# Performance work log

Hardware: AMD Instinct MI355X
Metric: run time of the kernel (lower is better)

Reference implementation:

```python
import jax, jax.numpy as jnp
import numpy as np

N_GRAPHS = 256
RATIO = 0.5


def setup_inputs() -> dict:
    key = jax.random.key(0)
    k0, k1, k2, k3, k4 = jax.random.split(key, 5)
    N, E, D = 100000, 1600000, 64
    x = jax.random.normal(k0, (N, D), dtype=jnp.float32)
    edge_index = jax.random.randint(k1, (2, E), 0, N, dtype=jnp.int32)
    batch = jnp.sort(jax.random.randint(k2, (N,), 0, N_GRAPHS, dtype=jnp.int32))
    # GraphConv(in_channels=64, out_channels=1) parameters
    w_rel = jax.random.normal(k3, (D,), dtype=jnp.float32) * 0.1
    b_rel = jnp.zeros((), dtype=jnp.float32)
    w_root = jax.random.normal(k4, (D,), dtype=jnp.float32) * 0.1
    return {"x": x, "edge_index": edge_index, "batch": batch,
            "w_rel": w_rel, "b_rel": b_rel, "w_root": w_root}


def reference(x, edge_index, batch, w_rel, b_rel, w_root):
    N = x.shape[0]
    src, dst = edge_index[0], edge_index[1]
    # GraphConv score: lin_rel(sum_{j in N(i)} x_j) + lin_root(x_i)
    agg = jax.ops.segment_sum(x[src], dst, num_segments=N)        # [N, D]
    score = jnp.tanh(agg @ w_rel + b_rel + x @ w_root)            # [N], SAGPool tanh
    # per-graph topk: keep k_g = ceil(ratio * n_g) highest-score nodes
    sizes = jax.ops.segment_sum(jnp.ones(N, jnp.int32), batch,
                                num_segments=N_GRAPHS)            # [G]
    k = jnp.ceil(RATIO * sizes.astype(jnp.float32)).astype(jnp.int32)
    starts = jnp.concatenate([jnp.zeros(1, jnp.int32),
                              jnp.cumsum(sizes)[:-1].astype(jnp.int32)])
    order = jnp.lexsort((-score, batch))                          # graph-major, score desc
    rank = jnp.arange(N, dtype=jnp.int32) - starts[batch[order]]  # rank within graph
    keep_sorted = rank < k[batch[order]]
    keep = jnp.zeros(N, dtype=bool).at[order].set(keep_sorted)
    # kept nodes are scaled by their tanh score; dropped nodes contribute 0
    w = jnp.where(keep, score, jnp.zeros_like(score))             # [N]
    num = jax.ops.segment_sum(x * w[:, None], batch, num_segments=N_GRAPHS)
    cnt = jax.ops.segment_sum(keep.astype(x.dtype), batch, num_segments=N_GRAPHS)
    return num / jnp.maximum(cnt, 1.0)[:, None]                   # global_mean_pool
```

## Files before the change

### kernel.cpp

```cpp
#include <hip/hip_runtime.h>

#define NGRAPHS 256
#define BINR   128
#define CAPB   3072
#define MAXB   1024
#define SBLK   512
#define CHUNKS 3328
#define NMAX   2048

__global__ __launch_bounds__(512) void kA_fused(
    const float* __restrict__ x,
    const int*   __restrict__ batch,
    const int*   __restrict__ ei,
    const float* __restrict__ w_rel,
    const float* __restrict__ w_root,
    float* __restrict__ p, float* __restrict__ r,
    int* __restrict__ starts, int* __restrict__ ends,
    int* __restrict__ cursor,
    unsigned* __restrict__ bucket,
    int N, int E, int chunkE, int NBINSP, int vecE)
{
    __shared__ __align__(16) unsigned stage[CHUNKS];
    __shared__ unsigned short sbin[CHUNKS];
    __shared__ int hist[MAXB];
    int tid = threadIdx.x;

    if ((int)blockIdx.x < SBLK) {
        if (E <= 0) return;
        for (int b = tid; b < NBINSP; b += 512) hist[b] = 0;
        __syncthreads();
        int beg = (int)blockIdx.x * chunkE;
        int end = min(beg + chunkE, E);
        int cnt = (end > beg) ? (end - beg) : 0;
        if (vecE) {
            const int4* s4 = (const int4*)ei;
            const int4* d4 = (const int4*)(ei + E);
            for (int i = (beg >> 2) + tid; i < (end >> 2); i += 512) {
                int4 d = d4[i];
                int4 s = s4[i];
                int o = (i << 2) - beg;
                int b0 = d.x >> 7, b1 = d.y >> 7, b2 = d.z >> 7, b3 = d.w >> 7;
                stage[o + 0] = ((unsigned)s.x << 7) | (unsigned)(d.x & 127);
                stage[o + 1] = ((unsigned)s.y << 7) | (unsigned)(d.y & 127);
                stage[o + 2] = ((unsigned)s.z << 7) | (unsigned)(d.z & 127);
                stage[o + 3] = ((unsigned)s.w << 7) | (unsigned)(d.w & 127);
                sbin[o + 0] = (unsigned short)b0;
                sbin[o + 1] = (unsigned short)b1;
                sbin[o + 2] = (unsigned short)b2;
                sbin[o + 3] = (unsigned short)b3;
                atomicAdd(&hist[b0], 1);
                atomicAdd(&hist[b1], 1);
                atomicAdd(&hist[b2], 1);
                atomicAdd(&hist[b3], 1);
            }
        } else {
            for (int i = beg + tid; i < end; i += 512) {
                int s = ei[i];
                int d = ei[E + i];
                int b = d >> 7;
                int o = i - beg;
                stage[o] = ((unsigned)s << 7) | (unsigned)(d & 127);
                sbin[o]  = (unsigned short)b;
                atomicAdd(&hist[b], 1);
            }
        }
        __syncthreads();
        for (int b = tid; b < NBINSP; b += 512) {
            int h = hist[b];
            hist[b] = (h > 0) ? b * CAPB + atomicAdd(&cursor[b], h) : 0;
        }
        __syncthreads();
        for (int o = tid; o < cnt; o += 512) {
            int b   = sbin[o];
            int pos = atomicAdd(&hist[b], 1);
            if (pos < (b + 1) * CAPB) bucket[pos] = stage[o];
        }
        return;
    }

    int row = ((int)blockIdx.x - SBLK) * 32 + (tid >> 4);
    int fq  = tid & 15;
    if (row >= N) return;
    if (fq == 0) {
        int b = batch[row];
        if (row == 0) {
            for (int g = 0; g < b; ++g) { starts[g] = 0; ends[g] = 0; }
            starts[b] = 0;
        } else {
            int bp = batch[row - 1];
            if (bp != b) {
                ends[bp] = row;
                for (int g = bp + 1; g < b; ++g) { starts[g] = row; ends[g] = row; }
                starts[b] = row;
            }
        }
        if (row == N - 1) {
            ends[b] = N;
            for (int g = b + 1; g < NGRAPHS; ++g) { starts[g] = N; ends[g] = N; }
        }
    }
    float4 v  = *(const float4*)(x + (size_t)row * 64 + fq * 4);
    float4 wr = ((const float4*)w_rel)[fq];
    float4 wo = ((const float4*)w_root)[fq];
    float a = v.x * wr.x + v.y * wr.y + v.z * wr.z + v.w * wr.w;
    float c = v.x * wo.x + v.y * wo.y + v.z * wo.z + v.w * wo.w;
    a += __shfl_down(a, 8); c += __shfl_down(c, 8);
    a += __shfl_down(a, 4); c += __shfl_down(c, 4);
    a += __shfl_down(a, 2); c += __shfl_down(c, 2);
    a += __shfl_down(a, 1); c += __shfl_down(c, 1);
    if (fq == 0) { p[row] = a; r[row] = c; }
}

__global__ __launch_bounds__(512) void kB_score(
    const unsigned* __restrict__ bucket,
    const int* __restrict__ cursor,
    const float* __restrict__ p,
    const float* __restrict__ r,
    const float* __restrict__ brel,
    float* __restrict__ score, int N)
{
    __shared__ float acc[BINR];
    int tid = threadIdx.x;
    int b   = blockIdx.x;
    if (tid < BINR) acc[tid] = 0.0f;
    __syncthreads();
    int lo  = b * CAPB;
    int cnt = min(cursor[b], CAPB);
    const uint4* bk4 = (const uint4*)(bucket + lo);
    int quart = cnt >> 2;
    for (int e = tid; e < quart; e += 512) {
        uint4 u = bk4[e];
        float v0 = p[u.x >> 7], v1 = p[u.y >> 7];
        float v2 = p[u.z >> 7], v3 = p[u.w >> 7];
        atomicAdd(&acc[u.x & 127u], v0);
        atomicAdd(&acc[u.y & 127u], v1);
        atomicAdd(&acc[u.z & 127u], v2);
        atomicAdd(&acc[u.w & 127u], v3);
    }
    int tail = cnt & 3;
    if (tid < tail) {
        unsigned u = bucket[lo + (quart << 2) + tid];
        atomicAdd(&acc[u & 127u], p[u >> 7]);
    }
    __syncthreads();
    int node = b * BINR + tid;
    if (tid < BINR && node < N)
        score[node] = tanhf(acc[tid] + brel[0] + r[node]);
}

__global__ __launch_bounds__(256) void kZ_zero(float* __restrict__ a, int N)
{
    int i = blockIdx.x * 256 + threadIdx.x;
    if (i < N) a[i] = 0.0f;
}
__global__ __launch_bounds__(256) void k2_scatter(
    const int* __restrict__ ei, const float* __restrict__ p,
    float* aggdot, int E)
{
    int i = blockIdx.x * 256 + threadIdx.x;
    if (i < E) unsafeAtomicAdd(&aggdot[ei[E + i]], p[ei[i]]);
}
__global__ __launch_bounds__(256) void kS_score(
    const float* __restrict__ aggdot, const float* __restrict__ r,
    const float* __restrict__ brel, float* __restrict__ score, int N)
{
    int i = blockIdx.x * 256 + threadIdx.x;
    if (i < N) score[i] = tanhf(aggdot[i] + brel[0] + r[i]);
}

__global__ __launch_bounds__(512) void k4_pool(
    const float* __restrict__ x,
    const float* __restrict__ score,
    const int* __restrict__ starts,
    const int* __restrict__ ends,
    float* __restrict__ out)
{
    __shared__ __align__(16) float sc[NMAX];
    __shared__ int   kidx[NMAX / 2 + 64];
    __shared__ float kw[NMAX / 2 + 64];
    __shared__ float accs[8][64][4];
    __shared__ int   pctr;

    int g   = blockIdx.x;
    int tid = threadIdx.x;
    int start = starts[g];
    int n     = ends[g] - start;
    if (n > NMAX) n = NMAX;
    int k = (n + 1) >> 1;
    if (tid == 0) pctr = 0;

    for (int i = tid; i < n; i += 512) sc[i] = score[start + i];
    __syncthreads();

    int n4 = n & ~3;
    for (int i = tid; i < n; i += 512) {
        float si = sc[i];
        int rank = 0;
        int j = 0;
        for (; j < n4; j += 4) {
            float4 s4 = *(const float4*)&sc[j];
            rank += (s4.x > si) || (s4.x == si && (j + 0) < i);
            rank += (s4.y > si) || (s4.y == si && (j + 1) < i);
            rank += (s4.z > si) || (s4.z == si && (j + 2) < i);
            rank += (s4.w > si) || (s4.w == si && (j + 3) < i);
        }
        for (; j < n; ++j) {
            float sj = sc[j];
            rank += (sj > si) || (sj == si && j < i);
        }
        if (rank < k) {
            int pos = atomicAdd(&pctr, 1);
            kidx[pos] = i;
            kw[pos]   = si;
        }
    }
    __syncthreads();
    int k32 = (k + 31) & ~31;
    for (int e = k + tid; e < k32; e += 512) { kidx[e] = 0; kw[e] = 0.0f; }
    __syncthreads();

    int wg   = tid >> 6;
    int lane = tid & 63;
    int rgrp = lane >> 4;
    int fq   = lane & 15;
    float a0 = 0.0f, a1 = 0.0f, a2 = 0.0f, a3 = 0.0f;
    #pragma unroll 2
    for (int e = wg * 4 + rgrp; e < k32; e += 32) {
        float wv = kw[e];
        int row  = start + kidx[e];
        const float4 v = *(const float4*)(x + (size_t)row * 64 + fq * 4);
        a0 += v.x * wv; a1 += v.y * wv; a2 += v.z * wv; a3 += v.w * wv;
    }
    accs[wg][lane][0] = a0; accs[wg][lane][1] = a1;
    accs[wg][lane][2] = a2; accs[wg][lane][3] = a3;
    __syncthreads();
    if (tid < 64) {
        float sum = 0.0f;
        #pragma unroll
        for (int gg = 0; gg < 8; ++gg)
            #pragma unroll
            for (int rg = 0; rg < 4; ++rg)
                sum += accs[gg][rg * 16 + (tid >> 2)][tid & 3];
        out[(size_t)g * 64 + tid] = sum / fmaxf((float)k, 1.0f);
    }
}

extern "C" void kernel_launch(void* const* d_in, const int* in_sizes, int n_in,
                              void* d_out, int out_size, void* d_ws, size_t ws_size,
                              hipStream_t stream) {
    const float* x      = (const float*)d_in[0];
    const int*   ei     = (const int*)  d_in[1];
    const int*   batch  = (const int*)  d_in[2];
    const float* w_rel  = (const float*)d_in[3];
    const float* b_rel  = (const float*)d_in[4];
    const float* w_root = (const float*)d_in[5];
    float* out = (float*)d_out;

    int N = in_sizes[2];
    int E = in_sizes[1] / 2;
    int NBINS  = (N + BINR - 1) / BINR;
    int NBINSP = (NBINS + 15) & ~15;
    int chunkE = (((E + SBLK - 1) / SBLK) + 3) & ~3;
    int vecE   = ((E & 3) == 0);
    int dotblks = (N + 31) / 32;

    float* p      = (float*)d_ws;
    float* r      = p + (size_t)N;
    float* score  = r + (size_t)N;
    int*   starts = (int*)(score + (size_t)N);
    int*   ends   = starts + NGRAPHS;
    int*   cursor = ends + NGRAPHS;
    size_t boff = (size_t)3 * N + 2 * NGRAPHS + MAXB;
    boff = (boff + 3) & ~(size_t)3;
    unsigned* bucket = (unsigned*)d_ws + boff;
    size_t need = (boff + (size_t)NBINSP * CAPB) * 4;

    bool binned = (need <= ws_size) && (NBINSP <= MAXB)
                  && (chunkE <= CHUNKS) && (N <= (1 << 24)) && (E > 0);

    if (binned) {
        hipMemsetAsync(cursor, 0, MAXB * sizeof(int), stream);
        kA_fused<<<SBLK + dotblks, 512, 0, stream>>>(
            x, batch, ei, w_rel, w_root, p, r, starts, ends, cursor, bucket,
            N, E, chunkE, NBINSP, vecE);
        kB_score<<<NBINS, 512, 0, stream>>>(bucket, cursor, p, r, b_rel, score, N);
    } else {
        float* aggdot = (float*)bucket;
        kA_fused<<<SBLK + dotblks, 512, 0, stream>>>(
            x, batch, ei, w_rel, w_root, p, r, starts, ends, cursor, bucket,
            N, 0, 0, NBINSP, vecE);
        kZ_zero<<<(N + 255) / 256, 256, 0, stream>>>(aggdot, N);
        k2_scatter<<<(E + 255) / 256, 256, 0, stream>>>(ei, p, aggdot, E);
        kS_score<<<(N + 255) / 256, 256, 0, stream>>>(aggdot, r, b_rel, score, N);
    }
    k4_pool<<<NGRAPHS, 512, 0, stream>>>(x, score, starts, ends, out);
}
```

Before: 137.2 us.

## Replace staged global-cursor binning with per-block fixed-capacity bucket cells

The edge binning no longer stages edges in shared memory and reserves space through global atomic cursors. Each source block now writes edges straight into its own fixed-capacity cell (24 slots) per destination bin and records a count per (bin, block). This removes the LDS staging pass, the global atomics and the cursor memset. The score kernel then has each thread walk one block's cell for its bin. In exchange the bucket buffer is much larger and the score-kernel reads are less coalesced, and any edges that overflow a cell are dropped, so a guard limits the binned path to about 8 expected edges per cell.

```diff
diff --git a/kernel.cpp b/kernel.cpp
--- a/kernel.cpp
+++ b/kernel.cpp
@@ -2,10 +2,10 @@
 
 #define NGRAPHS 256
 #define BINR   128
-#define CAPB   3072
 #define MAXB   1024
 #define SBLK   512
-#define CHUNKS 3328
+#define CAPC   24
+#define BINCAP (SBLK * CAPC)
 #define NMAX   2048
 
 __global__ __launch_bounds__(512) void kA_fused(
@@ -16,69 +16,57 @@
     const float* __restrict__ w_root,
     float* __restrict__ p, float* __restrict__ r,
     int* __restrict__ starts, int* __restrict__ ends,
-    int* __restrict__ cursor,
+    int* __restrict__ Ct,
     unsigned* __restrict__ bucket,
     int N, int E, int chunkE, int NBINSP, int vecE)
 {
-    __shared__ __align__(16) unsigned stage[CHUNKS];
-    __shared__ unsigned short sbin[CHUNKS];
-    __shared__ int hist[MAXB];
+    __shared__ int cur[MAXB];
     int tid = threadIdx.x;
-
-    if ((int)blockIdx.x < SBLK) {
+    int blk = (int)blockIdx.x;
+
+    if (blk < SBLK) {
         if (E <= 0) return;
-        for (int b = tid; b < NBINSP; b += 512) hist[b] = 0;
+        for (int b = tid; b < NBINSP; b += 512) cur[b] = 0;
         __syncthreads();
-        int beg = (int)blockIdx.x * chunkE;
+        int beg = blk * chunkE;
         int end = min(beg + chunkE, E);
-        int cnt = (end > beg) ? (end - beg) : 0;
+        unsigned cellbase = (unsigned)blk * CAPC;
         if (vecE) {
             const int4* s4 = (const int4*)ei;
             const int4* d4 = (const int4*)(ei + E);
             for (int i = (beg >> 2) + tid; i < (end >> 2); i += 512) {
                 int4 d = d4[i];
                 int4 s = s4[i];
-                int o = (i << 2) - beg;
-                int b0 = d.x >> 7, b1 = d.y >> 7, b2 = d.z >> 7, b3 = d.w >> 7;
-                stage[o + 0] = ((unsigned)s.x << 7) | (unsigned)(d.x & 127);
-                stage[o + 1] = ((unsigned)s.y << 7) | (unsigned)(d.y & 127);
-                stage[o + 2] = ((unsigned)s.z << 7) | (unsigned)(d.z & 127);
-                stage[o + 3] = ((unsigned)s.w << 7) | (unsigned)(d.w & 127);
-                sbin[o + 0] = (unsigned short)b0;
-                sbin[o + 1] = (unsigned short)b1;
-                sbin[o + 2] = (unsigned short)b2;
-                sbin[o + 3] = (unsigned short)b3;
-                atomicAdd(&hist[b0], 1);
-                atomicAdd(&hist[b1], 1);
-                atomicAdd(&hist[b2], 1);
-                atomicAdd(&hist[b3], 1);
+                int b0 = d.x >> 7, p0 = atomicAdd(&cur[b0], 1);
+                if (p0 < CAPC) bucket[(size_t)b0 * BINCAP + cellbase + p0] =
+                    ((unsigned)s.x << 7) | (unsigned)(d.x & 127);
+                int b1 = d.y >> 7, p1 = atomicAdd(&cur[b1], 1);
+                if (p1 < CAPC) bucket[(size_t)b1 * BINCAP + cellbase + p1] =
+                    ((unsigned)s.y << 7) | (unsigned)(d.y & 127);
+                int b2 = d.z >> 7, p2 = atomicAdd(&cur[b2], 1);
+                if (p2 < CAPC) bucket[(size_t)b2 * BINCAP + cellbase + p2] =
+                    ((unsigned)s.z << 7) | (unsigned)(d.z & 127);
+                int b3 = d.w >> 7, p3 = atomicAdd(&cur[b3], 1);
+                if (p3 < CAPC) bucket[(size_t)b3 * BINCAP + cellbase + p3] =
+                    ((unsigned)s.w << 7) | (unsigned)(d.w & 127);
             }
         } else {
             for (int i = beg + tid; i < end; i += 512) {
                 int s = ei[i];
                 int d = ei[E + i];
                 int b = d >> 7;
-                int o = i - beg;
-                stage[o] = ((unsigned)s << 7) | (unsigned)(d & 127);
-                sbin[o]  = (unsigned short)b;
-                atomicAdd(&hist[b], 1);
+                int pos = atomicAdd(&cur[b], 1);
+                if (pos < CAPC) bucket[(size_t)b * BINCAP + cellbase + pos] =
+                    ((unsigned)s << 7) | (unsigned)(d & 127);
             }
         }
         __syncthreads();
-        for (int b = tid; b < NBINSP; b += 512) {
-            int h = hist[b];
-            hist[b] = (h > 0) ? b * CAPB + atomicAdd(&cursor[b], h) : 0;
-        }
-        __syncthreads();
-        for (int o = tid; o < cnt; o += 512) {
-            int b   = sbin[o];
-            int pos = atomicAdd(&hist[b], 1);
-            if (pos < (b + 1) * CAPB) bucket[pos] = stage[o];
-        }
+        for (int b = tid; b < NBINSP; b += 512)
+            Ct[(size_t)b * SBLK + blk] = min(cur[b], CAPC);
         return;
     }
 
-    int row = ((int)blockIdx.x - SBLK) * 32 + (tid >> 4);
+    int row = (blk - SBLK) * 32 + (tid >> 4);
     int fq  = tid & 15;
     if (row >= N) return;
     if (fq == 0) {
@@ -113,7 +101,7 @@
 
 __global__ __launch_bounds__(512) void kB_score(
     const unsigned* __restrict__ bucket,
-    const int* __restrict__ cursor,
+    const int* __restrict__ Ct,
     const float* __restrict__ p,
     const float* __restrict__ r,
     const float* __restrict__ brel,
@@ -124,22 +112,10 @@
     int b   = blockIdx.x;
     if (tid < BINR) acc[tid] = 0.0f;
     __syncthreads();
-    int lo  = b * CAPB;
-    int cnt = min(cursor[b], CAPB);
-    const uint4* bk4 = (const uint4*)(bucket + lo);
-    int quart = cnt >> 2;
-    for (int e = tid; e < quart; e += 512) {
-        uint4 u = bk4[e];
-        float v0 = p[u.x >> 7], v1 = p[u.y >> 7];
-        float v2 = p[u.z >> 7], v3 = p[u.w >> 7];
-        atomicAdd(&acc[u.x & 127u], v0);
-        atomicAdd(&acc[u.y & 127u], v1);
-        atomicAdd(&acc[u.z & 127u], v2);
-        atomicAdd(&acc[u.w & 127u], v3);
-    }
-    int tail = cnt & 3;
-    if (tid < tail) {
-        unsigned u = bucket[lo + (quart << 2) + tid];
+    int c = Ct[(size_t)b * SBLK + tid];
+    size_t base = (size_t)b * BINCAP + (size_t)tid * CAPC;
+    for (int j = 0; j < c; ++j) {
+        unsigned u = bucket[base + j];
         atomicAdd(&acc[u & 127u], p[u >> 7]);
     }
     __syncthreads();
@@ -269,25 +245,26 @@
     float* score  = r + (size_t)N;
     int*   starts = (int*)(score + (size_t)N);
     int*   ends   = starts + NGRAPHS;
-    int*   cursor = ends + NGRAPHS;
-    size_t boff = (size_t)3 * N + 2 * NGRAPHS + MAXB;
-    boff = (boff + 3) & ~(size_t)3;
+    size_t coff = (size_t)3 * N + 2 * NGRAPHS;
+    coff = (coff + 3) & ~(size_t)3;
+    int* Ct = (int*)d_ws + coff;
+    size_t boff = coff + (size_t)NBINSP * SBLK;
     unsigned* bucket = (unsigned*)d_ws + boff;
-    size_t need = (boff + (size_t)NBINSP * CAPB) * 4;
-
-    bool binned = (need <= ws_size) && (NBINSP <= MAXB)
-                  && (chunkE <= CHUNKS) && (N <= (1 << 24)) && (E > 0);
+    size_t need = (boff + (size_t)NBINSP * BINCAP) * 4;
+
+    double lam = (NBINS > 0) ? (double)chunkE / (double)NBINS : 0.0;
+    bool binned = (need <= ws_size) && (NBINSP <= MAXB) && (E > 0)
+                  && (N <= (1 << 17)) && (lam <= 8.0);
 
     if (binned) {
-        hipMemsetAsync(cursor, 0, MAXB * sizeof(int), stream);
         kA_fused<<<SBLK + dotblks, 512, 0, stream>>>(
-            x, batch, ei, w_rel, w_root, p, r, starts, ends, cursor, bucket,
+            x, batch, ei, w_rel, w_root, p, r, starts, ends, Ct, bucket,
             N, E, chunkE, NBINSP, vecE);
-        kB_score<<<NBINS, 512, 0, stream>>>(bucket, cursor, p, r, b_rel, score, N);
+        kB_score<<<NBINS, 512, 0, stream>>>(bucket, Ct, p, r, b_rel, score, N);
     } else {
-        float* aggdot = (float*)bucket;
+        float* aggdot = (float*)Ct;
         kA_fused<<<SBLK + dotblks, 512, 0, stream>>>(
-            x, batch, ei, w_rel, w_root, p, r, starts, ends, cursor, bucket,
+            x, batch, ei, w_rel, w_root, p, r, starts, ends, Ct, bucket,
             N, 0, 0, NBINSP, vecE);
         kZ_zero<<<(N + 255) / 256, 256, 0, stream>>>(aggdot, N);
         k2_scatter<<<(E + 255) / 256, 256, 0, stream>>>(ei, p, aggdot, E);
```

Result: no change. 138.4 us (+0.9%).
